# Kernel optimization log

Hardware: AMD Instinct MI355X
Metric: run time of the kernel (lower is better)

The kernel has to match this reference:

```python
import jax, jax.numpy as jnp
import numpy as np

D = 64        # feature dim (== units, required by residual add)
B = 131072    # batch (collocation points)
P = D * (D - 1) // 2  # number of strictly-upper-triangular pairs = 2016

# Static pair indices (i < j), matching row-major boolean_mask of r[:,None] < r
_I, _J = np.triu_indices(D, k=1)
IDX_I = jnp.asarray(_I)
IDX_J = jnp.asarray(_J)


def setup_inputs() -> dict:
    key = jax.random.key(0)
    k1, k2 = jax.random.split(key)
    x = jax.random.normal(k1, (B, D), dtype=jnp.float32)
    # w_init = tf.random_normal_initializer() defaults to stddev=0.05
    w1 = jax.random.normal(k2, (P, D), dtype=jnp.float32) * 0.05
    return {"x": x, "w1": w1}


def reference(x, w1):
    # Pairwise products x_i * x_j for i < j only (avoids full [B, D*D] tensor).
    prod = x[:, IDX_I] * x[:, IDX_J]          # [B, P]
    return jnp.matmul(prod, w1) + x           # [B, D]
```

## Files before the change

### kernel.cpp

```cpp
#include <hip/hip_runtime.h>
#include <hip/hip_bf16.h>
#include <stdint.h>

typedef unsigned short ushort_t;
typedef __attribute__((ext_vector_type(8))) _Float16 half8_t;
typedef __attribute__((ext_vector_type(4))) _Float16 half4_t;
typedef __attribute__((ext_vector_type(2))) _Float16 half2_t;
typedef __attribute__((ext_vector_type(4))) float f32x4;

#define DIM 64
#define NGROUP 280
#define NSTEP 70
#define BM 128
#define XS_STRIDE 72

__device__ inline void gid_to_ij(int gid, int& i_out, int& j0_out) {
    int cum = 0;
    i_out = 0; j0_out = 0;
    #pragma unroll
    for (int ii = 0; ii < 64; ++ii) {
        int jstart = ((ii + 1) >> 3) << 3;
        int ng = (64 - jstart) >> 3;
        if (gid >= cum && gid < cum + ng) {
            i_out = ii;
            j0_out = jstart + (gid - cum) * 8;
        }
        cum += ng;
    }
}

__global__ void wpack_kernel(const float* __restrict__ w1,
                             _Float16* __restrict__ w_h,
                             uint32_t* __restrict__ idx_tab) {
    int id = blockIdx.x * 256 + threadIdx.x;
    if (id >= NGROUP * 8 * 64) return;
    int e    = id & 7;
    int lane = (id >> 3) & 63;
    int st   = id >> 9;
    int s    = st >> 2;
    int t    = st & 3;
    int g    = lane >> 4;
    int c    = lane & 15;
    int n    = t * 16 + c;
    int gid  = s * 4 + g;

    int i, j0;
    gid_to_ij(gid, i, j0);
    int j = j0 + e;
    float w = 0.0f;
    if (j > i) {
        int p = i * DIM - (i * (i + 1)) / 2 + (j - i - 1);
        w = w1[p * DIM + n];
    }
    w_h[id] = (_Float16)w;
    if (e == 0 && c == 0 && t == 0) idx_tab[gid] = (uint32_t)i | ((uint32_t)j0 << 8);
}

__global__ __launch_bounds__(256, 4)
void prodres_kernel(const float* __restrict__ x,
                    const _Float16* __restrict__ w_h,
                    const uint32_t* __restrict__ idx_tab,
                    float* __restrict__ out) {
    __shared__ _Float16 xs[BM * XS_STRIDE];
    __shared__ uint32_t idx_s[NGROUP];

    const int t    = threadIdx.x;
    const int lane = t & 63;
    const int wave = t >> 6;
    const long brow = (long)blockIdx.x * BM;

    #pragma unroll
    for (int it = 0; it < 8; ++it) {
        int row = it * 16 + (t >> 4);
        int c   = (t & 15) * 4;
        float4 v = *reinterpret_cast<const float4*>(x + (brow + row) * DIM + c);
        half4_t h;
        h[0] = (_Float16)v.x; h[1] = (_Float16)v.y;
        h[2] = (_Float16)v.z; h[3] = (_Float16)v.w;
        *reinterpret_cast<half4_t*>(&xs[row * XS_STRIDE + c]) = h;
    }
    for (int ii = t; ii < NGROUP; ii += 256) idx_s[ii] = idx_tab[ii];
    __syncthreads();

    const int lrow = lane & 15;
    const int g    = lane >> 4;

    f32x4 acc[2][4];
    #pragma unroll
    for (int m = 0; m < 2; ++m)
        #pragma unroll
        for (int n = 0; n < 4; ++n) {
            f32x4 z = {0.f, 0.f, 0.f, 0.f};
            acc[m][n] = z;
        }

    const half8_t* wp = reinterpret_cast<const half8_t*>(w_h);

    #pragma unroll 2
    for (int s = 0; s < NSTEP; ++s) {
        half8_t bh[4];
        #pragma unroll
        for (int n = 0; n < 4; ++n)
            bh[n] = wp[(s * 4 + n) * 64 + lane];

        uint32_t ij = idx_s[s * 4 + g];
        int i  = (int)(ij & 0xffu);
        int j0 = (int)((ij >> 8) & 0xffu);

        half8_t ah[2];
        #pragma unroll
        for (int m = 0; m < 2; ++m) {
            const _Float16* xr = &xs[(wave * 32 + m * 16 + lrow) * XS_STRIDE];
            _Float16 xi = xr[i];
            half2_t xi2 = {xi, xi};
            half8_t xj = *reinterpret_cast<const half8_t*>(xr + j0);
            half2_t* ap = reinterpret_cast<half2_t*>(&ah[m]);
            const half2_t* jp = reinterpret_cast<const half2_t*>(&xj);
            #pragma unroll
            for (int e2 = 0; e2 < 4; ++e2) ap[e2] = xi2 * jp[e2];
        }

        #pragma unroll
        for (int m = 0; m < 2; ++m)
            #pragma unroll
            for (int n = 0; n < 4; ++n)
                acc[m][n] = __builtin_amdgcn_mfma_f32_16x16x32_f16(ah[m], bh[n], acc[m][n], 0, 0, 0);
    }

    #pragma unroll
    for (int m = 0; m < 2; ++m)
        #pragma unroll
        for (int q = 0; q < 4; ++q) {
            long row = brow + wave * 32 + m * 16 + g * 4 + q;
            #pragma unroll
            for (int n = 0; n < 4; ++n) {
                int col = n * 16 + lrow;
                out[row * DIM + col] = acc[m][n][q] + x[row * DIM + col];
            }
        }
}

extern "C" void kernel_launch(void* const* d_in, const int* in_sizes, int n_in,
                              void* d_out, int out_size, void* d_ws, size_t ws_size,
                              hipStream_t stream) {
    const float* x  = (const float*)d_in[0];
    const float* w1 = (const float*)d_in[1];
    float* out = (float*)d_out;

    const size_t WELEMS = (size_t)NGROUP * 8 * 64;
    _Float16* w_h = (_Float16*)d_ws;
    uint32_t* idx_tab = (uint32_t*)(w_h + WELEMS);

    int b_total = in_sizes[0] / DIM;

    wpack_kernel<<<(NGROUP * 8 * 64 + 255) / 256, 256, 0, stream>>>(w1, w_h, idx_tab);
    prodres_kernel<<<b_total / BM, 256, 0, stream>>>(x, w_h, idx_tab, out);
}
```

Measured before the change: 122.0 us.

## Double per-block rows, prefetch next step operands, reuse LDS x for residual

Raises the block tile from 128 to 256 rows, so each wave computes a 64x64 output tile and every B fragment loaded from global feeds twice as many MFMAs. Software-pipelines the main loop by loading the next step's weight fragments and x operands from LDS before the current MFMAs run, to hide load latency. The residual add now reads the fp16 copy of x already in LDS instead of re-reading fp32 x from global, which drops precision of the residual term. Register pressure rises and occupancy is lowered to 2 blocks per SIMD, and LDS use per block doubles.

```diff
diff --git a/kernel.cpp b/kernel.cpp
--- a/kernel.cpp
+++ b/kernel.cpp
@@ -11,7 +11,7 @@
 #define DIM 64
 #define NGROUP 280
 #define NSTEP 70
-#define BM 128
+#define BM 256
 #define XS_STRIDE 72
 
 __device__ inline void gid_to_ij(int gid, int& i_out, int& j0_out) {
@@ -56,7 +56,7 @@
     if (e == 0 && c == 0 && t == 0) idx_tab[gid] = (uint32_t)i | ((uint32_t)j0 << 8);
 }
 
-__global__ __launch_bounds__(256, 4)
+__global__ __launch_bounds__(256, 2)
 void prodres_kernel(const float* __restrict__ x,
                     const _Float16* __restrict__ w_h,
                     const uint32_t* __restrict__ idx_tab,
@@ -70,7 +70,7 @@
     const long brow = (long)blockIdx.x * BM;
 
     #pragma unroll
-    for (int it = 0; it < 8; ++it) {
+    for (int it = 0; it < 16; ++it) {
         int row = it * 16 + (t >> 4);
         int c   = (t & 15) * 4;
         float4 v = *reinterpret_cast<const float4*>(x + (brow + row) * DIM + c);
@@ -85,9 +85,14 @@
     const int lrow = lane & 15;
     const int g    = lane >> 4;
 
-    f32x4 acc[2][4];
+    const _Float16* xr[4];
     #pragma unroll
-    for (int m = 0; m < 2; ++m)
+    for (int m = 0; m < 4; ++m)
+        xr[m] = &xs[(wave * 64 + m * 16 + lrow) * XS_STRIDE];
+
+    f32x4 acc[4][4];
+    #pragma unroll
+    for (int m = 0; m < 4; ++m)
         #pragma unroll
         for (int n = 0; n < 4; ++n) {
             f32x4 z = {0.f, 0.f, 0.f, 0.f};
@@ -96,46 +101,73 @@
 
     const half8_t* wp = reinterpret_cast<const half8_t*>(w_h);
 
+    half8_t bcur[4];
+    #pragma unroll
+    for (int n = 0; n < 4; ++n) bcur[n] = wp[n * 64 + lane];
+
+    uint32_t ij0 = idx_s[g];
+    int i_c  = (int)(ij0 & 0xffu);
+    int j0_c = (int)((ij0 >> 8) & 0xffu);
+    _Float16 xi_c[4];
+    half8_t  xj_c[4];
+    #pragma unroll
+    for (int m = 0; m < 4; ++m) {
+        xi_c[m] = xr[m][i_c];
+        xj_c[m] = *reinterpret_cast<const half8_t*>(xr[m] + j0_c);
+    }
+
     #pragma unroll 2
     for (int s = 0; s < NSTEP; ++s) {
-        half8_t bh[4];
+        int sn = (s + 1 < NSTEP) ? s + 1 : s;
+
+        half8_t bnxt[4];
         #pragma unroll
         for (int n = 0; n < 4; ++n)
-            bh[n] = wp[(s * 4 + n) * 64 + lane];
+            bnxt[n] = wp[(sn * 4 + n) * 64 + lane];
 
-        uint32_t ij = idx_s[s * 4 + g];
-        int i  = (int)(ij & 0xffu);
-        int j0 = (int)((ij >> 8) & 0xffu);
+        uint32_t ijn = idx_s[sn * 4 + g];
+        int i_n  = (int)(ijn & 0xffu);
+        int j0_n = (int)((ijn >> 8) & 0xffu);
+        _Float16 xi_n[4];
+        half8_t  xj_n[4];
+        #pragma unroll
+        for (int m = 0; m < 4; ++m) {
+            xi_n[m] = xr[m][i_n];
+            xj_n[m] = *reinterpret_cast<const half8_t*>(xr[m] + j0_n);
+        }
 
-        half8_t ah[2];
+        half8_t ah[4];
         #pragma unroll
-        for (int m = 0; m < 2; ++m) {
-            const _Float16* xr = &xs[(wave * 32 + m * 16 + lrow) * XS_STRIDE];
-            _Float16 xi = xr[i];
-            half2_t xi2 = {xi, xi};
-            half8_t xj = *reinterpret_cast<const half8_t*>(xr + j0);
+        for (int m = 0; m < 4; ++m) {
+            half2_t xi2 = {xi_c[m], xi_c[m]};
             half2_t* ap = reinterpret_cast<half2_t*>(&ah[m]);
-            const half2_t* jp = reinterpret_cast<const half2_t*>(&xj);
+            const half2_t* jp = reinterpret_cast<const half2_t*>(&xj_c[m]);
             #pragma unroll
             for (int e2 = 0; e2 < 4; ++e2) ap[e2] = xi2 * jp[e2];
         }
 
         #pragma unroll
-        for (int m = 0; m < 2; ++m)
+        for (int m = 0; m < 4; ++m)
             #pragma unroll
             for (int n = 0; n < 4; ++n)
-                acc[m][n] = __builtin_amdgcn_mfma_f32_16x16x32_f16(ah[m], bh[n], acc[m][n], 0, 0, 0);
+                acc[m][n] = __builtin_amdgcn_mfma_f32_16x16x32_f16(ah[m], bcur[n], acc[m][n], 0, 0, 0);
+
+        #pragma unroll
+        for (int n = 0; n < 4; ++n) bcur[n] = bnxt[n];
+        #pragma unroll
+        for (int m = 0; m < 4; ++m) { xi_c[m] = xi_n[m]; xj_c[m] = xj_n[m]; }
     }
 
     #pragma unroll
-    for (int m = 0; m < 2; ++m)
+    for (int m = 0; m < 4; ++m)
         #pragma unroll
         for (int q = 0; q < 4; ++q) {
-            long row = brow + wave * 32 + m * 16 + g * 4 + q;
+            int lr = wave * 64 + m * 16 + g * 4 + q;
+            long row = brow + lr;
             #pragma unroll
             for (int n = 0; n < 4; ++n) {
                 int col = n * 16 + lrow;
-                out[row * DIM + col] = acc[m][n][q] + x[row * DIM + col];
+                out[row * DIM + col] = acc[m][n][q] + (float)xs[lr * XS_STRIDE + col];
             }
         }
 }
```

After: 113.2 us. -7.3%, faster.

## Switch to 32x32x16 MFMA with register-resident x rows and compile-time pair schedule

Applied to the files above, without the earlier changes.

Replaces the 16x16x32 MFMA loop with 32x32x16 MFMAs over 16-wide j-blocks, cutting padded K groups from 280 to 156. Each wave now covers 64 rows, so the block tile grows to 256 rows. Each lane keeps its x row as fp16 pairs in registers, and a constexpr schedule unrolled through templates makes the pair indices compile-time constants, removing per-step LDS reads and the index table. Weight fragments are prefetched two steps ahead with triple buffering. The cost is heavy register use, with launch bounds lowered to 2 blocks per SIMD, which reduces occupancy, and a large fully unrolled code body.

```diff
diff --git a/kernel.cpp b/kernel.cpp
--- a/kernel.cpp
+++ b/kernel.cpp
@@ -2,140 +2,186 @@
 #include <hip/hip_bf16.h>
 #include <stdint.h>
 
-typedef unsigned short ushort_t;
 typedef __attribute__((ext_vector_type(8))) _Float16 half8_t;
 typedef __attribute__((ext_vector_type(4))) _Float16 half4_t;
 typedef __attribute__((ext_vector_type(2))) _Float16 half2_t;
-typedef __attribute__((ext_vector_type(4))) float f32x4;
+typedef __attribute__((ext_vector_type(16))) float f32x16;
 
 #define DIM 64
-#define NGROUP 280
-#define NSTEP 70
-#define BM 128
-#define XS_STRIDE 72
-
-__device__ inline void gid_to_ij(int gid, int& i_out, int& j0_out) {
-    int cum = 0;
-    i_out = 0; j0_out = 0;
-    #pragma unroll
+#define NKH 156
+#define NSTEP 78
+#define BM 256
+#define XS_STRIDE 68
+
+struct SchedT { int i[NKH]; int j0[NKH]; };
+constexpr SchedT make_sched() {
+    SchedT s{};
+    int n = 0;
+    for (int i = 0; i < 64; ++i)
+        for (int jb = (i + 1) >> 4; jb < 4; ++jb) { s.i[n] = i; s.j0[n] = jb * 16; ++n; }
+    return s;
+}
+constexpr SchedT SC = make_sched();
+
+__device__ inline void kg_to_ij(int kg, int& io, int& jo) {
+    int cum = 0; io = 0; jo = 0;
     for (int ii = 0; ii < 64; ++ii) {
-        int jstart = ((ii + 1) >> 3) << 3;
-        int ng = (64 - jstart) >> 3;
-        if (gid >= cum && gid < cum + ng) {
-            i_out = ii;
-            j0_out = jstart + (gid - cum) * 8;
-        }
-        cum += ng;
+        int jb0 = (ii + 1) >> 4;
+        int nb = 4 - jb0;
+        if (kg >= cum && kg < cum + nb) { io = ii; jo = (jb0 + (kg - cum)) * 16; }
+        cum += nb;
     }
 }
 
 __global__ void wpack_kernel(const float* __restrict__ w1,
-                             _Float16* __restrict__ w_h,
-                             uint32_t* __restrict__ idx_tab) {
+                             _Float16* __restrict__ w_h) {
     int id = blockIdx.x * 256 + threadIdx.x;
-    if (id >= NGROUP * 8 * 64) return;
+    if (id >= NSTEP * 4 * 64 * 8) return;
     int e    = id & 7;
     int lane = (id >> 3) & 63;
-    int st   = id >> 9;
-    int s    = st >> 2;
-    int t    = st & 3;
-    int g    = lane >> 4;
-    int c    = lane & 15;
-    int n    = t * 16 + c;
-    int gid  = s * 4 + g;
-
+    int c    = id >> 9;
+    int s    = c >> 2;
+    int t    = (c >> 1) & 1;
+    int h    = c & 1;
+    int kg   = s * 2 + h;
     int i, j0;
-    gid_to_ij(gid, i, j0);
-    int j = j0 + e;
+    kg_to_ij(kg, i, j0);
+    int j = j0 + ((lane >> 5) << 3) + e;
+    int n = t * 32 + (lane & 31);
     float w = 0.0f;
     if (j > i) {
         int p = i * DIM - (i * (i + 1)) / 2 + (j - i - 1);
         w = w1[p * DIM + n];
     }
     w_h[id] = (_Float16)w;
-    if (e == 0 && c == 0 && t == 0) idx_tab[gid] = (uint32_t)i | ((uint32_t)j0 << 8);
-}
-
-__global__ __launch_bounds__(256, 4)
+}
+
+template<int KG, int MT>
+__device__ __forceinline__ half8_t aprod(const uint32_t (&xr)[2][32], bool hi) {
+    constexpr int I  = SC.i[KG];
+    constexpr int J0 = SC.j0[KG];
+    constexpr int DI = I >> 1;
+    constexpr int DJ = J0 >> 1;
+    uint32_t dwi = hi ? xr[MT][DI ^ 4] : xr[MT][DI];
+    half2_t hv = __builtin_bit_cast(half2_t, dwi);
+    _Float16 xi = hv[I & 1];
+    half2_t xi2 = {xi, xi};
+    half8_t r;
+    half2_t* rp = reinterpret_cast<half2_t*>(&r);
+    #pragma unroll
+    for (int e2 = 0; e2 < 4; ++e2) {
+        half2_t xj = __builtin_bit_cast(half2_t, xr[MT][DJ + e2]);
+        rp[e2] = xi2 * xj;
+    }
+    return r;
+}
+
+template<int S>
+struct Step {
+    static __device__ __forceinline__ void run(const uint32_t (&xr)[2][32],
+                                               half8_t (&b)[3][4],
+                                               f32x16 (&acc)[2][2],
+                                               const half8_t* wl, bool hi) {
+        constexpr int SP = (S + 2 < NSTEP) ? S + 2 : NSTEP - 1;
+        #pragma unroll
+        for (int t = 0; t < 4; ++t)
+            b[(S + 2) % 3][t] = wl[(SP * 4 + t) * 64];
+
+        half8_t ah0[2], ah1[2];
+        ah0[0] = aprod<S * 2 + 0, 0>(xr, hi);
+        ah0[1] = aprod<S * 2 + 0, 1>(xr, hi);
+        ah1[0] = aprod<S * 2 + 1, 0>(xr, hi);
+        ah1[1] = aprod<S * 2 + 1, 1>(xr, hi);
+
+        #pragma unroll
+        for (int mt = 0; mt < 2; ++mt)
+            #pragma unroll
+            for (int nt = 0; nt < 2; ++nt)
+                acc[mt][nt] = __builtin_amdgcn_mfma_f32_32x32x16_f16(
+                    ah0[mt], b[S % 3][nt * 2 + 0], acc[mt][nt], 0, 0, 0);
+        #pragma unroll
+        for (int mt = 0; mt < 2; ++mt)
+            #pragma unroll
+            for (int nt = 0; nt < 2; ++nt)
+                acc[mt][nt] = __builtin_amdgcn_mfma_f32_32x32x16_f16(
+                    ah1[mt], b[S % 3][nt * 2 + 1], acc[mt][nt], 0, 0, 0);
+
+        Step<S + 1>::run(xr, b, acc, wl, hi);
+    }
+};
+template<>
+struct Step<NSTEP> {
+    static __device__ __forceinline__ void run(const uint32_t (&)[2][32], half8_t (&)[3][4],
+                                               f32x16 (&)[2][2], const half8_t*, bool) {}
+};
+
+__global__ __launch_bounds__(256, 2)
 void prodres_kernel(const float* __restrict__ x,
                     const _Float16* __restrict__ w_h,
-                    const uint32_t* __restrict__ idx_tab,
                     float* __restrict__ out) {
     __shared__ _Float16 xs[BM * XS_STRIDE];
-    __shared__ uint32_t idx_s[NGROUP];
 
     const int t    = threadIdx.x;
     const int lane = t & 63;
     const int wave = t >> 6;
+    const bool hi  = (lane >> 5) & 1;
     const long brow = (long)blockIdx.x * BM;
 
     #pragma unroll
-    for (int it = 0; it < 8; ++it) {
+    for (int it = 0; it < 16; ++it) {
         int row = it * 16 + (t >> 4);
         int c   = (t & 15) * 4;
         float4 v = *reinterpret_cast<const float4*>(x + (brow + row) * DIM + c);
-        half4_t h;
-        h[0] = (_Float16)v.x; h[1] = (_Float16)v.y;
-        h[2] = (_Float16)v.z; h[3] = (_Float16)v.w;
-        *reinterpret_cast<half4_t*>(&xs[row * XS_STRIDE + c]) = h;
-    }
-    for (int ii = t; ii < NGROUP; ii += 256) idx_s[ii] = idx_tab[ii];
+        half4_t hq;
+        hq[0] = (_Float16)v.x; hq[1] = (_Float16)v.y;
+        hq[2] = (_Float16)v.z; hq[3] = (_Float16)v.w;
+        *reinterpret_cast<half4_t*>(&xs[row * XS_STRIDE + c]) = hq;
+    }
     __syncthreads();
 
-    const int lrow = lane & 15;
-    const int g    = lane >> 4;
-
-    f32x4 acc[2][4];
-    #pragma unroll
-    for (int m = 0; m < 2; ++m)
-        #pragma unroll
-        for (int n = 0; n < 4; ++n) {
-            f32x4 z = {0.f, 0.f, 0.f, 0.f};
-            acc[m][n] = z;
+    uint32_t xr[2][32];
+    #pragma unroll
+    for (int mt = 0; mt < 2; ++mt) {
+        int row = wave * 64 + mt * 32 + (lane & 31);
+        const uint32_t* rp = reinterpret_cast<const uint32_t*>(&xs[row * XS_STRIDE]);
+        #pragma unroll
+        for (int c2 = 0; c2 < 16; ++c2) {
+            int src = (2 * c2) ^ (hi ? 4 : 0);
+            uint64_t v = *reinterpret_cast<const uint64_t*>(rp + src);
+            xr[mt][2 * c2]     = (uint32_t)v;
+            xr[mt][2 * c2 + 1] = (uint32_t)(v >> 32);
         }
-
-    const half8_t* wp = reinterpret_cast<const half8_t*>(w_h);
-
-    #pragma unroll 2
-    for (int s = 0; s < NSTEP; ++s) {
-        half8_t bh[4];
-        #pragma unroll
-        for (int n = 0; n < 4; ++n)
-            bh[n] = wp[(s * 4 + n) * 64 + lane];
-
-        uint32_t ij = idx_s[s * 4 + g];
-        int i  = (int)(ij & 0xffu);
-        int j0 = (int)((ij >> 8) & 0xffu);
-
-        half8_t ah[2];
-        #pragma unroll
-        for (int m = 0; m < 2; ++m) {
-            const _Float16* xr = &xs[(wave * 32 + m * 16 + lrow) * XS_STRIDE];
-            _Float16 xi = xr[i];
-            half2_t xi2 = {xi, xi};
-            half8_t xj = *reinterpret_cast<const half8_t*>(xr + j0);
-            half2_t* ap = reinterpret_cast<half2_t*>(&ah[m]);
-            const half2_t* jp = reinterpret_cast<const half2_t*>(&xj);
-            #pragma unroll
-            for (int e2 = 0; e2 < 4; ++e2) ap[e2] = xi2 * jp[e2];
-        }
-
-        #pragma unroll
-        for (int m = 0; m < 2; ++m)
-            #pragma unroll
-            for (int n = 0; n < 4; ++n)
-                acc[m][n] = __builtin_amdgcn_mfma_f32_16x16x32_f16(ah[m], bh[n], acc[m][n], 0, 0, 0);
-    }
-
-    #pragma unroll
-    for (int m = 0; m < 2; ++m)
-        #pragma unroll
-        for (int q = 0; q < 4; ++q) {
-            long row = brow + wave * 32 + m * 16 + g * 4 + q;
-            #pragma unroll
-            for (int n = 0; n < 4; ++n) {
-                int col = n * 16 + lrow;
-                out[row * DIM + col] = acc[m][n][q] + x[row * DIM + col];
+    }
+
+    f32x16 acc[2][2];
+    #pragma unroll
+    for (int mt = 0; mt < 2; ++mt)
+        #pragma unroll
+        for (int nt = 0; nt < 2; ++nt)
+            #pragma unroll
+            for (int q = 0; q < 16; ++q) acc[mt][nt][q] = 0.0f;
+
+    const half8_t* wl = reinterpret_cast<const half8_t*>(w_h) + lane;
+    half8_t b[3][4];
+
+    #pragma unroll
+    for (int tt = 0; tt < 4; ++tt) b[0][tt] = wl[tt * 64];
+    #pragma unroll
+    for (int tt = 0; tt < 4; ++tt) b[1][tt] = wl[(4 + tt) * 64];
+
+    Step<0>::run(xr, b, acc, wl, hi);
+
+    const int hib = hi ? 4 : 0;
+    #pragma unroll
+    for (int mt = 0; mt < 2; ++mt)
+        #pragma unroll
+        for (int q = 0; q < 16; ++q) {
+            int rit = (q & 3) + 8 * (q >> 2) + hib;
+            long row = brow + wave * 64 + mt * 32 + rit;
+            #pragma unroll
+            for (int nt = 0; nt < 2; ++nt) {
+                int col = nt * 32 + (lane & 31);
+                out[row * DIM + col] = acc[mt][nt][q] + x[row * DIM + col];
             }
         }
 }
@@ -147,12 +193,10 @@
     const float* w1 = (const float*)d_in[1];
     float* out = (float*)d_out;
 
-    const size_t WELEMS = (size_t)NGROUP * 8 * 64;
     _Float16* w_h = (_Float16*)d_ws;
-    uint32_t* idx_tab = (uint32_t*)(w_h + WELEMS);
 
     int b_total = in_sizes[0] / DIM;
 
-    wpack_kernel<<<(NGROUP * 8 * 64 + 255) / 256, 256, 0, stream>>>(w1, w_h, idx_tab);
-    prodres_kernel<<<b_total / BM, 256, 0, stream>>>(x, w_h, idx_tab, out);
-}
+    wpack_kernel<<<(NSTEP * 4 * 64 * 8 + 255) / 256, 256, 0, stream>>>(w1, w_h);
+    prodres_kernel<<<b_total / BM, 256, 0, stream>>>(x, w_h, out);
+}
```

Result: slower. 126.2 us (+3.4%).
